# Performance work log

Hardware: AMD Instinct MI355X
Metric: run time of the kernel (lower is better)

The kernel has to match this reference:

```python
import jax, jax.numpy as jnp
import numpy as np

NUM_CLASS = 22  # restypes_with_x_and_gap


def setup_inputs() -> dict:
    key = jax.random.key(0)
    k1, k2, k3, k4 = jax.random.split(key, 4)
    b, m, n, c = 1, 128, 256, NUM_CLASS
    variant = jax.random.randint(k1, (b, m, n), 0, c)              # int variant sequences
    variant_mask = jnp.ones((b, m, n), dtype=jnp.float32)
    eij = jax.random.normal(k2, (b, n, n, c, c), dtype=jnp.float32) * 0.1  # Potts couplings wij
    ei = jax.random.normal(k3, (b, n, c), dtype=jnp.float32) * 0.1         # fields bi
    mask_vec = jnp.ones((c,), dtype=jnp.float32).at[-1].set(0.0)   # mask out gap '-' class
    sigma = jnp.ones((1,), dtype=jnp.float32)                      # prior_w=1.0, task_num=1
    return {"variant": variant, "variant_mask": variant_mask, "eij": eij,
            "ei": ei, "mask_vec": mask_vec, "sigma": sigma}


def reference(variant, variant_mask, eij, ei, mask_vec, sigma):
    c = mask_vec.shape[0]
    onehot = jax.nn.one_hot(variant, c, dtype=eij.dtype)           # [b,m,n,c]
    # fold class mask into couplings, then Potts energy per position/class
    em = eij * mask_vec                                            # [b,i,j,c,d]
    hi = jnp.einsum('bmjd,bijcd->bmic', onehot, em)                # [b,m,i,c]
    motifs = ei[:, None] + hi                                      # [b,m,i,c]
    # log_softmax=False branch: pick the logit of the active class per position
    logits = jnp.einsum('bmic,bmic->bmi', motifs, onehot)          # [b,m,i]
    # eval path: delta vs reference variant (index 0), sum-pooled, scaled by sigma
    vm = variant_mask[..., None]                                   # [b,m,i,1]
    vm = vm * vm[:, :1]
    vlogit = logits - logits[:, :1]                                # [b,m,i]
    pooled = jnp.sum(vlogit[..., None] * vm, axis=-2)              # [b,m,task_num]
    variant_logit = sigma * pooled
    return motifs, logits, variant_logit
```

## Files before the change

kernel.cpp:

```cpp
#include <hip/hip_runtime.h>

#define NC    22
#define NROW  (NC*NC)
#define NJ    256
#define NI    256
#define NM    128
#define NQJ   4
#define JQ    (NJ/NQJ)
#define SS    8
#define ROWDW 16
#define JROW  (NC*ROWDW)
#define WBUF  (2*JROW)
#define VTS   132
#define SLAB  (NI*NM*NC)
#define NRB   (SLAB/1024)

typedef __attribute__((ext_vector_type(8))) short short8;
typedef __attribute__((ext_vector_type(4))) float f32x4;

__device__ __forceinline__ uint32_t bf16rne(float x) {
    uint32_t u = __float_as_uint(x);
    u += 0x7FFFu + ((u >> 16) & 1u);
    return u >> 16;
}

__device__ __forceinline__ uint32_t pk_bf16(float lo, float hi) {
    uint32_t r;
    asm("v_cvt_pk_bf16_f32 %0, %1, %2" : "=v"(r) : "v"(lo), "v"(hi));
    return r;
}

__global__ __launch_bounds__(256, 4) void potts_mfma(
    const int*   __restrict__ variant,
    const float* __restrict__ eij,
    const float* __restrict__ mask_vec,
    float*       __restrict__ part)
{
    const int i    = blockIdx.x;
    const int jq   = blockIdx.y;
    const int tid  = threadIdx.x;
    const int lane = tid & 63;
    const int w    = tid >> 6;
    const int q    = lane >> 4;
    const int nl   = lane & 15;
    const int kb   = q * 4;

    __shared__ uint32_t      tile[4][WBUF * 2];
    __shared__ unsigned char vt8[JQ * VTS];
    __shared__ uint32_t      patTab[32];

    if (tid < 32) {
        const uint32_t mb = (tid < NC) ? bf16rne(mask_vec[tid]) : 0u;
        patTab[tid] = mb << ((tid & 1) << 4);
    }
    for (int p = tid; p < JQ * NM; p += 256) {
        const int jl = p & 63, m = p >> 6;
        vt8[jl * VTS + m] = (unsigned char)variant[m * NJ + jq * JQ + jl];
    }
    {
        uint32_t* wbase = tile[w];
        for (int p = lane; p < 2 * 2 * NC * 5; p += 64) {
            const int b = p / (2 * NC * 5), r = p % (2 * NC * 5);
            const int jl = r / (NC * 5), r2 = r % (NC * 5);
            wbase[b * WBUF + jl * JROW + (r2 / 5) * ROWDW + 11 + r2 % 5] = 0;
        }
    }
    __syncthreads();

    int  l0[4], l1[4];
    bool act[4];
    #pragma unroll
    for (int r = 0; r < 4; ++r) {
        const int f4 = r * 64 + lane;
        act[r] = (f4 < 242);
        const int fc = act[r] ? f4 : 0;
        const int jl = fc / 121, r4 = fc % 121;
        const int f2a = 2 * r4, f2b = f2a + 1;
        l0[r] = jl * JROW + (f2a / 11) * ROWDW + f2a % 11;
        l1[r] = jl * JROW + (f2b / 11) * ROWDW + f2b % 11;
    }

    const float4* gsrc = (const float4*)eij
                       + (size_t)(i * NJ + jq * JQ + w * 16) * (NROW / 4);

    const int c1   = 16 + nl;
    const int off0 = nl * ROWDW + kb;
    const int off1 = (c1 < NC ? c1 : 0) * ROWDW + kb;

    f32x4 acc[8][2];
    #pragma unroll
    for (int t = 0; t < 8; ++t) {
        acc[t][0] = (f32x4){0.f, 0.f, 0.f, 0.f};
        acc[t][1] = (f32x4){0.f, 0.f, 0.f, 0.f};
    }

    float4 pf[4];
    #pragma unroll
    for (int r = 0; r < 4; ++r)
        if (act[r]) pf[r] = gsrc[r * 64 + lane];

    for (int s = 0; s < SS; ++s) {
        uint32_t* buf = tile[w] + (s & 1) * WBUF;

        #pragma unroll
        for (int r = 0; r < 4; ++r) {
            if (act[r]) {
                const float4 v = pf[r];
                buf[l0[r]] = pk_bf16(v.x, v.y);
                buf[l1[r]] = pk_bf16(v.z, v.w);
            }
        }
        if (s + 1 < SS) {
            const float4* gn = gsrc + (size_t)(s + 1) * 242;
            #pragma unroll
            for (int r = 0; r < 4; ++r)
                if (act[r]) pf[r] = gn[r * 64 + lane];
        }

        #pragma unroll
        for (int jj = 0; jj < 2; ++jj) {
            const uint32_t* jrow = buf + jj * JROW;
            const short8 bf0 = *(const short8*)(jrow + off0);
            const short8 bf1 = *(const short8*)(jrow + off1);

            const unsigned char* vrow = &vt8[(w * 16 + s * 2 + jj) * VTS];
            #pragma unroll
            for (int t = 0; t < 8; ++t) {
                const int      va = vrow[t * 16 + nl];
                const uint32_t pa = patTab[va];
                const int      ha = va >> 1;
                union { uint32_t u[4]; short8 s; } fa;
                #pragma unroll
                for (int tt = 0; tt < 4; ++tt)
                    fa.u[tt] = (ha == kb + tt) ? pa : 0u;
                acc[t][0] = __builtin_amdgcn_mfma_f32_16x16x32_bf16(fa.s, bf0, acc[t][0], 0, 0, 0);
                acc[t][1] = __builtin_amdgcn_mfma_f32_16x16x32_bf16(fa.s, bf1, acc[t][1], 0, 0, 0);
            }
        }
    }

    __syncthreads();
    float* red   = (float*)&tile[0][0];
    float* myred = red + (w & 1) * (NM * NC);
    if (w < 2) {
        #pragma unroll
        for (int t = 0; t < 8; ++t)
            #pragma unroll
            for (int tt = 0; tt < 4; ++tt) {
                const int m = t * 16 + kb + tt;
                myred[m * NC + nl] = acc[t][0][tt];
                if (c1 < NC) myred[m * NC + c1] = acc[t][1][tt];
            }
    }
    __syncthreads();
    if (w >= 2) {
        #pragma unroll
        for (int t = 0; t < 8; ++t)
            #pragma unroll
            for (int tt = 0; tt < 4; ++tt) {
                const int m = t * 16 + kb + tt;
                myred[m * NC + nl] += acc[t][0][tt];
                if (c1 < NC) myred[m * NC + c1] += acc[t][1][tt];
            }
    }
    __syncthreads();
    float* pbase = part + ((size_t)jq * NI + i) * (NM * NC);
    #pragma unroll
    for (int k = 0; k < 11; ++k) {
        const int p = k * 256 + tid;
        pbase[p] = red[p] + red[NM * NC + p];
    }
}

__global__ __launch_bounds__(1024) void potts_reduce(
    const float* __restrict__ part,
    const int*   __restrict__ variant,
    const float* __restrict__ ei,
    float*       __restrict__ out_motifs,
    float*       __restrict__ out_logits)
{
    const int idx = blockIdx.x * 1024 + threadIdx.x;
    float s = 0.f;
    #pragma unroll
    for (int qq = 0; qq < NQJ; ++qq)
        s += part[(size_t)qq * SLAB + idx];

    const int i = idx / (NM * NC);
    const int r = idx - i * (NM * NC);
    const int m = r / NC;
    const int c = r - m * NC;

    const float v = s + ei[i * NC + c];
    out_motifs[((size_t)m * NI + i) * NC + c] = v;
    if (c == variant[m * NJ + i])
        out_logits[m * NI + i] = v;
}

__global__ __launch_bounds__(64) void potts_pool(
    const float* __restrict__ logits,
    const float* __restrict__ vmask,
    const float* __restrict__ sigma,
    float*       __restrict__ out_vl)
{
    const int m    = blockIdx.x;
    const int lane = threadIdx.x;
    float s = 0.f;
    #pragma unroll
    for (int qq = 0; qq < 4; ++qq) {
        const int i = lane + 64 * qq;
        const float vl = logits[m * NI + i] - logits[i];
        s += vl * vmask[m * NI + i] * vmask[i];
    }
    #pragma unroll
    for (int off = 32; off > 0; off >>= 1)
        s += __shfl_down(s, off, 64);
    if (lane == 0) out_vl[m] = sigma[0] * s;
}

extern "C" void kernel_launch(void* const* d_in, const int* in_sizes, int n_in,
                              void* d_out, int out_size, void* d_ws, size_t ws_size,
                              hipStream_t stream) {
    const int*   variant  = (const int*)  d_in[0];
    const float* vmask    = (const float*)d_in[1];
    const float* eij      = (const float*)d_in[2];
    const float* ei       = (const float*)d_in[3];
    const float* mask_vec = (const float*)d_in[4];
    const float* sigma    = (const float*)d_in[5];

    float* out        = (float*)d_out;
    float* out_motifs = out;
    float* out_logits = out_motifs + NM * NI * NC;
    float* out_vl     = out_logits + NM * NI;

    float* part = (float*)d_ws;

    dim3 gridA(NI, NQJ);
    potts_mfma<<<gridA, 256, 0, stream>>>(variant, eij, mask_vec, part);
    potts_reduce<<<NRB, 1024, 0, stream>>>(part, variant, ei,
                                           out_motifs, out_logits);
    potts_pool<<<NM, 64, 0, stream>>>(out_logits, vmask, sigma, out_vl);
}
```

Measured before the change: 210.4 us.

## Stream couplings via direct global-to-LDS loads with 4-slot pipeline, restructure reduce

The main kernel now copies fp32 eij rows straight into LDS with global_load_lds, using a 4-slot ring and a prefetch distance of two rows. Conversion to bf16 moves to the MFMA B-fragment read, replacing the register prefetch and pack-store staging. The variant table is repacked so each lane fetches its 8 class indices with two 32-bit loads. The reduce kernel is restructured to one block per i, with each thread reading 11 contiguous classes. This cuts LDS staging work and register pressure, but the reduce kernel's global accesses now use a 44-byte stride and coalesce less well.

Result: slower. 226.2 us (+7.5%).

```diff
diff --git a/kernel.cpp b/kernel.cpp
--- a/kernel.cpp
+++ b/kernel.cpp
@@ -7,13 +7,10 @@
 #define NM    128
 #define NQJ   4
 #define JQ    (NJ/NQJ)
-#define SS    8
-#define ROWDW 16
-#define JROW  (NC*ROWDW)
-#define WBUF  (2*JROW)
-#define VTS   132
+#define JPW   16
+#define SLOTF 496
+#define NSL   4
 #define SLAB  (NI*NM*NC)
-#define NRB   (SLAB/1024)
 
 typedef __attribute__((ext_vector_type(8))) short short8;
 typedef __attribute__((ext_vector_type(4))) float f32x4;
@@ -29,6 +26,16 @@
     asm("v_cvt_pk_bf16_f32 %0, %1, %2" : "=v"(r) : "v"(lo), "v"(hi));
     return r;
 }
+
+__device__ __forceinline__ void gload_lds16(const void* g, void* l) {
+    __builtin_amdgcn_global_load_lds(
+        (const __attribute__((address_space(1))) void*)g,
+        (__attribute__((address_space(3))) void*)l, 16, 0, 0);
+}
+
+#define WAITV(n) asm volatile("s_waitcnt vmcnt(" #n ")" ::: "memory")
+
+union u32x4s8 { uint32_t u[4]; short8 s; };
 
 __global__ __launch_bounds__(256, 4) void potts_mfma(
     const int*   __restrict__ variant,
@@ -45,47 +52,31 @@
     const int nl   = lane & 15;
     const int kb   = q * 4;
 
-    __shared__ uint32_t      tile[4][WBUF * 2];
-    __shared__ unsigned char vt8[JQ * VTS];
+    __shared__ float         slots[4][NSL][SLOTF];
+    __shared__ unsigned char vtp[JQ * NM];
     __shared__ uint32_t      patTab[32];
 
     if (tid < 32) {
         const uint32_t mb = (tid < NC) ? bf16rne(mask_vec[tid]) : 0u;
         patTab[tid] = mb << ((tid & 1) << 4);
     }
+    if (tid < 4 * NSL * (SLOTF - 484)) {
+        const int ww = tid / (NSL * 12), r = tid % (NSL * 12);
+        slots[ww][r / 12][484 + r % 12] = 0.f;
+    }
     for (int p = tid; p < JQ * NM; p += 256) {
-        const int jl = p & 63, m = p >> 6;
-        vt8[jl * VTS + m] = (unsigned char)variant[m * NJ + jq * JQ + jl];
-    }
-    {
-        uint32_t* wbase = tile[w];
-        for (int p = lane; p < 2 * 2 * NC * 5; p += 64) {
-            const int b = p / (2 * NC * 5), r = p % (2 * NC * 5);
-            const int jl = r / (NC * 5), r2 = r % (NC * 5);
-            wbase[b * WBUF + jl * JROW + (r2 / 5) * ROWDW + 11 + r2 % 5] = 0;
-        }
-    }
-    __syncthreads();
-
-    int  l0[4], l1[4];
-    bool act[4];
-    #pragma unroll
-    for (int r = 0; r < 4; ++r) {
-        const int f4 = r * 64 + lane;
-        act[r] = (f4 < 242);
-        const int fc = act[r] ? f4 : 0;
-        const int jl = fc / 121, r4 = fc % 121;
-        const int f2a = 2 * r4, f2b = f2a + 1;
-        l0[r] = jl * JROW + (f2a / 11) * ROWDW + f2a % 11;
-        l1[r] = jl * JROW + (f2b / 11) * ROWDW + f2b % 11;
-    }
-
-    const float4* gsrc = (const float4*)eij
-                       + (size_t)(i * NJ + jq * JQ + w * 16) * (NROW / 4);
+        const int jl = p >> 7, mm = p & 127;
+        vtp[jl * 128 + (mm & 15) * 8 + (mm >> 4)] =
+            (unsigned char)variant[mm * NJ + jq * JQ + jl];
+    }
+    __syncthreads();
+
+    const float* gbase = eij + (size_t)(i * NJ + jq * JQ + w * JPW) * NROW;
 
     const int c1   = 16 + nl;
-    const int off0 = nl * ROWDW + kb;
-    const int off1 = (c1 < NC ? c1 : 0) * ROWDW + kb;
+    const int c1r  = (c1 < NC) ? c1 : 0;
+    const int fo0  = nl * NC + q * 8;
+    const int fo1  = c1r * NC + q * 8;
 
     f32x4 acc[8][2];
     #pragma unroll
@@ -94,53 +85,58 @@
         acc[t][1] = (f32x4){0.f, 0.f, 0.f, 0.f};
     }
 
-    float4 pf[4];
-    #pragma unroll
-    for (int r = 0; r < 4; ++r)
-        if (act[r]) pf[r] = gsrc[r * 64 + lane];
-
-    for (int s = 0; s < SS; ++s) {
-        uint32_t* buf = tile[w] + (s & 1) * WBUF;
+    #pragma unroll
+    for (int J = 0; J < 2; ++J) {
+        const float* g = gbase + (size_t)J * NROW;
+        float* l = &slots[w][J][0];
+        gload_lds16(g + lane * 4, l);
+        gload_lds16(g + 228 + lane * 4, l + 228);
+    }
+
+    #pragma unroll
+    for (int j = 0; j < JPW; ++j) {
+        if (j + 2 < JPW) {
+            const float* g = gbase + (size_t)(j + 2) * NROW;
+            float* l = &slots[w][(j + 2) & (NSL - 1)][0];
+            gload_lds16(g + lane * 4, l);
+            gload_lds16(g + 228 + lane * 4, l + 228);
+        }
+        if (j < 14)      WAITV(4);
+        else if (j < 15) WAITV(2);
+        else             WAITV(0);
+
+        const float* jb = &slots[w][j & (NSL - 1)][0];
+
+        const float2* r0 = (const float2*)jb + (fo0 >> 1);
+        const float2* r1 = (const float2*)jb + (fo1 >> 1);
+        const float2 x0 = r0[0], x1 = r0[1], x2 = r0[2], x3 = r0[3];
+        const float2 y0 = r1[0], y1 = r1[1], y2 = r1[2], y3 = r1[3];
+        u32x4s8 B0, B1;
+        B0.u[0] = pk_bf16(x0.x, x0.y);  B0.u[1] = pk_bf16(x1.x, x1.y);
+        B0.u[2] = pk_bf16(x2.x, x2.y);  B0.u[3] = pk_bf16(x3.x, x3.y);
+        B1.u[0] = pk_bf16(y0.x, y0.y);  B1.u[1] = pk_bf16(y1.x, y1.y);
+        B1.u[2] = pk_bf16(y2.x, y2.y);  B1.u[3] = pk_bf16(y3.x, y3.y);
+
+        const uint32_t* vj = (const uint32_t*)&vtp[(w * JPW + j) * 128 + nl * 8];
+        const uint32_t vlo = vj[0], vhi = vj[1];
 
         #pragma unroll
-        for (int r = 0; r < 4; ++r) {
-            if (act[r]) {
-                const float4 v = pf[r];
-                buf[l0[r]] = pk_bf16(v.x, v.y);
-                buf[l1[r]] = pk_bf16(v.z, v.w);
-            }
+        for (int t = 0; t < 8; ++t) {
+            const uint32_t vd = (t < 4) ? vlo : vhi;
+            const int      va = (vd >> ((t & 3) * 8)) & 0xFF;
+            const uint32_t pa = patTab[va];
+            const int      ha = va >> 1;
+            u32x4s8 A;
+            #pragma unroll
+            for (int tt = 0; tt < 4; ++tt)
+                A.u[tt] = (ha == kb + tt) ? pa : 0u;
+            acc[t][0] = __builtin_amdgcn_mfma_f32_16x16x32_bf16(A.s, B0.s, acc[t][0], 0, 0, 0);
+            acc[t][1] = __builtin_amdgcn_mfma_f32_16x16x32_bf16(A.s, B1.s, acc[t][1], 0, 0, 0);
         }
-        if (s + 1 < SS) {
-            const float4* gn = gsrc + (size_t)(s + 1) * 242;
-            #pragma unroll
-            for (int r = 0; r < 4; ++r)
-                if (act[r]) pf[r] = gn[r * 64 + lane];
-        }
-
-        #pragma unroll
-        for (int jj = 0; jj < 2; ++jj) {
-            const uint32_t* jrow = buf + jj * JROW;
-            const short8 bf0 = *(const short8*)(jrow + off0);
-            const short8 bf1 = *(const short8*)(jrow + off1);
-
-            const unsigned char* vrow = &vt8[(w * 16 + s * 2 + jj) * VTS];
-            #pragma unroll
-            for (int t = 0; t < 8; ++t) {
-                const int      va = vrow[t * 16 + nl];
-                const uint32_t pa = patTab[va];
-                const int      ha = va >> 1;
-                union { uint32_t u[4]; short8 s; } fa;
-                #pragma unroll
-                for (int tt = 0; tt < 4; ++tt)
-                    fa.u[tt] = (ha == kb + tt) ? pa : 0u;
-                acc[t][0] = __builtin_amdgcn_mfma_f32_16x16x32_bf16(fa.s, bf0, acc[t][0], 0, 0, 0);
-                acc[t][1] = __builtin_amdgcn_mfma_f32_16x16x32_bf16(fa.s, bf1, acc[t][1], 0, 0, 0);
-            }
-        }
-    }
-
-    __syncthreads();
-    float* red   = (float*)&tile[0][0];
+    }
+
+    __syncthreads();
+    float* red   = &slots[0][0][0];
     float* myred = red + (w & 1) * (NM * NC);
     if (w < 2) {
         #pragma unroll
@@ -172,28 +168,36 @@
     }
 }
 
-__global__ __launch_bounds__(1024) void potts_reduce(
+__global__ __launch_bounds__(256) void potts_reduce(
     const float* __restrict__ part,
     const int*   __restrict__ variant,
     const float* __restrict__ ei,
     float*       __restrict__ out_motifs,
     float*       __restrict__ out_logits)
 {
-    const int idx = blockIdx.x * 1024 + threadIdx.x;
-    float s = 0.f;
-    #pragma unroll
-    for (int qq = 0; qq < NQJ; ++qq)
-        s += part[(size_t)qq * SLAB + idx];
-
-    const int i = idx / (NM * NC);
-    const int r = idx - i * (NM * NC);
-    const int m = r / NC;
-    const int c = r - m * NC;
-
-    const float v = s + ei[i * NC + c];
-    out_motifs[((size_t)m * NI + i) * NC + c] = v;
-    if (c == variant[m * NJ + i])
-        out_logits[m * NI + i] = v;
+    const int i    = blockIdx.x;
+    const int tid  = threadIdx.x;
+    const int m    = tid & 127;
+    const int half = tid >> 7;
+    const int cc0  = half * 11;
+
+    const float* p0 = part + (((size_t)0 * NI + i) * NM + m) * NC + cc0;
+    const float* p1 = part + (((size_t)1 * NI + i) * NM + m) * NC + cc0;
+    const float* p2 = part + (((size_t)2 * NI + i) * NM + m) * NC + cc0;
+    const float* p3 = part + (((size_t)3 * NI + i) * NM + m) * NC + cc0;
+    const float* eirow = ei + i * NC;
+    float* mout = out_motifs + ((size_t)m * NI + i) * NC;
+    const int vi = variant[m * NJ + i];
+
+    float logit = 0.f;
+    #pragma unroll
+    for (int k = 0; k < 11; ++k) {
+        const float v = p0[k] + p1[k] + p2[k] + p3[k] + eirow[cc0 + k];
+        mout[cc0 + k] = v;
+        if (cc0 + k == vi) logit = v;
+    }
+    if (vi >= cc0 && vi < cc0 + 11)
+        out_logits[m * NI + i] = logit;
 }
 
 __global__ __launch_bounds__(64) void potts_pool(
@@ -236,7 +240,7 @@
 
     dim3 gridA(NI, NQJ);
     potts_mfma<<<gridA, 256, 0, stream>>>(variant, eij, mask_vec, part);
-    potts_reduce<<<NRB, 1024, 0, stream>>>(part, variant, ei,
-                                           out_motifs, out_logits);
+    potts_reduce<<<NI, 256, 0, stream>>>(part, variant, ei,
+                                         out_motifs, out_logits);
     potts_pool<<<NM, 64, 0, stream>>>(out_logits, vmask, sigma, out_vl);
 }
```
